# Kernel optimization log

Hardware: AMD Instinct MI355X
Metric: run time of the kernel (lower is better)

## Reference

```python
import jax, jax.numpy as jnp
import numpy as np

N = 100000
E = 1600000
L = 128   # latent_size
H = 128   # hidden_size
O = 128   # output_size


def setup_inputs() -> dict:
    key = jax.random.key(0)
    ks = jax.random.split(key, 16)
    s = 1.0 / np.sqrt(H)
    inp = {
        "z": jax.random.normal(ks[0], (N, L), dtype=jnp.float32),
        "edge_index": jax.random.randint(ks[1], (2, E), 0, N, dtype=jnp.int64),
        # LSTM params (torch order: i, f, g, o)
        "W_ih": jax.random.uniform(ks[2], (4 * H, L), jnp.float32, -s, s),
        "W_hh": jax.random.uniform(ks[3], (4 * H, H), jnp.float32, -s, s),
        "b_ih": jax.random.uniform(ks[4], (4 * H,), jnp.float32, -s, s),
        "b_hh": jax.random.uniform(ks[5], (4 * H,), jnp.float32, -s, s),
        # GCNConv weights (x @ W + b)
        "W1": jax.random.uniform(ks[6], (H, H), jnp.float32, -s, s),
        "b1": jnp.zeros((H,), jnp.float32),
        "W2": jax.random.uniform(ks[7], (H, H), jnp.float32, -s, s),
        "b2": jnp.zeros((H,), jnp.float32),
        # final Linear
        "W3": jax.random.uniform(ks[8], (O, H), jnp.float32, -s, s),
        "b3": jax.random.uniform(ks[9], (O,), jnp.float32, -s, s),
    }
    return inp


def _gcn_conv(x, W, b, src, dst, norm, n_nodes):
    # x: [N, H]; src/dst/norm: [E+N] (self-loops included)
    h = x @ W                                   # [N, H] transform first (H==H)
    msg = h[src] * norm[:, None]                # gather + edge scale
    out = jax.ops.segment_sum(msg, dst, num_segments=n_nodes)  # scatter-add
    return out + b


def _lstm_step(z, W_ih, W_hh, b_ih, b_hh):
    # single time-step, h0 = c0 = 0
    gates = z @ W_ih.T + (jnp.zeros((1, H), z.dtype) @ W_hh.T) + b_ih + b_hh
    i, f, g, o = jnp.split(gates, 4, axis=-1)
    c = jax.nn.sigmoid(i) * jnp.tanh(g)         # f * c0 == 0
    return jax.nn.sigmoid(o) * jnp.tanh(c)


def reference(z, edge_index, W_ih, W_hh, b_ih, b_hh, W1, b1, W2, b2, W3, b3):
    n = z.shape[0]
    # add self-loops (PyG GCNConv default)
    loop = jnp.arange(n, dtype=edge_index.dtype)
    src = jnp.concatenate([edge_index[0], loop])
    dst = jnp.concatenate([edge_index[1], loop])
    # symmetric normalization: deg from dst (incoming, incl. self-loop)
    deg = jax.ops.segment_sum(jnp.ones_like(dst, dtype=z.dtype), dst, num_segments=n)
    dinv = jnp.where(deg > 0, jax.lax.rsqrt(deg), 0.0)
    norm = dinv[src] * dinv[dst]

    h = _lstm_step(z, W_ih, W_hh, b_ih, b_hh)
    x = jax.nn.relu(_gcn_conv(h, W1, b1, src, dst, norm, n))
    x = _gcn_conv(x, W2, b2, src, dst, norm, n)
    return jax.nn.relu(x @ W3.T + b3)
```

## Files before the change

kernel.cpp:

```cpp
#include <hip/hip_runtime.h>
#include <math.h>

typedef __attribute__((ext_vector_type(8))) short short8;
typedef __attribute__((ext_vector_type(4))) float floatx4;

#define HDIM 128
#define NPB 256
#define BKMAX 1024
#define CHUNK 8192
#define STAGE_CAP 8192

__device__ __forceinline__ float bf2f(unsigned short u) {
    unsigned int x = ((unsigned int)u) << 16;
    float f;
    __builtin_memcpy(&f, &x, 4);
    return f;
}
__device__ __forceinline__ unsigned short f2bf(float f) {
    unsigned int x;
    __builtin_memcpy(&x, &f, 4);
    unsigned int r = (x + 0x7fffu + ((x >> 16) & 1u)) >> 16;
    return (unsigned short)r;
}
__device__ __forceinline__ void split1(float v, unsigned short& hi, unsigned short& lo) {
    unsigned int x;
    __builtin_memcpy(&x, &v, 4);
    hi = (unsigned short)(x >> 16);
    lo = f2bf(v - bf2f(hi));
}
__device__ __forceinline__ float fast_sigmoid(float x) {
    return 1.0f / (1.0f + __expf(-x));
}
__device__ __forceinline__ float fast_tanh(float x) {
    float ax = fabsf(x);
    float e = __expf(2.0f * ax);
    float t = 1.0f - 2.0f / (e + 1.0f);
    return copysignf(t, x);
}

__device__ __forceinline__ void gload_lds16(const void* g, void* lds) {
    __builtin_amdgcn_global_load_lds(
        (const __attribute__((address_space(1))) unsigned int*)g,
        (__attribute__((address_space(3))) unsigned int*)lds, 16, 0, 0);
}

__global__ void prep_weights_kernel(const float* __restrict__ Wih,
                                    const float* __restrict__ W1,
                                    const float* __restrict__ bih,
                                    const float* __restrict__ bhh,
                                    unsigned short* __restrict__ Wihh, unsigned short* __restrict__ Wihl,
                                    unsigned short* __restrict__ W1h,  unsigned short* __restrict__ W1l,
                                    float* __restrict__ bsum) {
    int i = blockIdx.x * 256 + threadIdx.x;
    unsigned short h, l;
    if (i < 65536) {
        split1(Wih[i], h, l);
        Wihh[i] = h; Wihl[i] = l;
    } else if (i < 81920) {
        int t = i - 65536, r = t >> 7, c = t & 127;
        split1(W1[r * HDIM + c], h, l);
        W1h[c * HDIM + r] = h; W1l[c * HDIM + r] = l;
    } else if (i < 82432) {
        int t = i - 81920;
        bsum[t] = bih[t] + bhh[t];
    }
}

__global__ void prep_w23_kernel(const float* __restrict__ W2,
                                const float* __restrict__ W3,
                                const float* __restrict__ b2,
                                const float* __restrict__ b3,
                                unsigned short* __restrict__ W23h,
                                unsigned short* __restrict__ W23l,
                                float* __restrict__ b23) {
    int i = blockIdx.x * 256 + threadIdx.x;
    if (i < 16384) {
        int n = i >> 7, k = i & 127;
        float s = 0.0f;
#pragma unroll 8
        for (int p = 0; p < 128; ++p)
            s += W2[k * HDIM + p] * W3[n * HDIM + p];
        unsigned short h, l;
        split1(s, h, l);
        W23h[n * HDIM + k] = h;
        W23l[n * HDIM + k] = l;
    } else if (i < 16512) {
        int n = i - 16384;
        float s = b3[n];
#pragma unroll 8
        for (int p = 0; p < 128; ++p)
            s += b2[p] * W3[n * HDIM + p];
        b23[n] = s;
    }
}

__global__ __launch_bounds__(256)
void bucket_hist_kernel(const int* __restrict__ ei, int* __restrict__ bcnt,
                        long E, int K) {
    __shared__ int h[BKMAX];
    const int tid = threadIdx.x;
    for (int i = tid; i < K; i += 256) h[i] = 0;
    __syncthreads();
    const long base = (long)blockIdx.x * CHUNK;
#pragma unroll
    for (int j = 0; j < CHUNK / 256; ++j) {
        long e = base + j * 256 + tid;
        if (e < E) atomicAdd(&h[((unsigned)ei[E + e]) >> 8], 1);
    }
    __syncthreads();
    for (int i = tid; i < K; i += 256) {
        int c = h[i];
        if (c) atomicAdd(&bcnt[i], c);
    }
}

__global__ __launch_bounds__(1024)
void scan_buckets_kernel(const int* __restrict__ bcnt, int* __restrict__ gbase,
                         int* __restrict__ gcur, int* __restrict__ offs,
                         int K, int N, int Etot) {
    __shared__ int buf[1024];
    const int t = threadIdx.x;
    const int v = (t < K) ? bcnt[t] : 0;
    buf[t] = v;
    __syncthreads();
    for (int off = 1; off < 1024; off <<= 1) {
        int x = buf[t];
        int y = (t >= off) ? buf[t - off] : 0;
        __syncthreads();
        buf[t] = x + y;
        __syncthreads();
    }
    if (t < K) { gbase[t] = buf[t] - v; gcur[t] = buf[t] - v; }
    if (t == 0) { gbase[K] = Etot; offs[N] = Etot; }
}

__global__ __launch_bounds__(256)
void pair_scatter_kernel(const int* __restrict__ ei, int* __restrict__ gcur,
                         unsigned int* __restrict__ pairs, long E, int K) {
    __shared__ int h[BKMAX];
    __shared__ int cur[BKMAX];
    const int tid = threadIdx.x;
    for (int i = tid; i < K; i += 256) h[i] = 0;
    __syncthreads();
    const long base = (long)blockIdx.x * CHUNK;
#pragma unroll
    for (int j = 0; j < CHUNK / 256; ++j) {
        long e = base + j * 256 + tid;
        if (e < E) atomicAdd(&h[((unsigned)ei[E + e]) >> 8], 1);
    }
    __syncthreads();
    for (int i = tid; i < K; i += 256) {
        int c = h[i];
        cur[i] = c ? atomicAdd(&gcur[i], c) : 0;
    }
    __syncthreads();
#pragma unroll
    for (int j = 0; j < CHUNK / 256; ++j) {
        long e = base + j * 256 + tid;
        if (e < E) {
            unsigned int s = (unsigned int)ei[e];
            unsigned int d = (unsigned int)ei[E + e];
            int b = d >> 8;
            int pos = atomicAdd(&cur[b], 1);
            pairs[pos] = s | ((d & (NPB - 1)) << 24);
        }
    }
}

__global__ __launch_bounds__(256)
void bucket_csr_kernel(const unsigned int* __restrict__ pairs, const int* __restrict__ gbase,
                       int* __restrict__ offs, float* __restrict__ dinv,
                       int* __restrict__ srclist, int N) {
    __shared__ int cnt[NPB];
    __shared__ int red[NPB];
    __shared__ int cur[NPB];
    __shared__ int stage[STAGE_CAP];
    const int tid = threadIdx.x;
    const int b = blockIdx.x;
    const int node0 = b << 8;
    const int nn = min(NPB, N - node0);
    const int ebeg = gbase[b];
    const int eend = gbase[b + 1];
    const int ne = eend - ebeg;

    cnt[tid] = 0;
    __syncthreads();
    for (int i = tid; i < ne; i += 256)
        atomicAdd(&cnt[pairs[ebeg + i] >> 24], 1);
    __syncthreads();
    const int myc = cnt[tid];
    red[tid] = myc;
    __syncthreads();
    for (int off = 1; off < NPB; off <<= 1) {
        int x = red[tid];
        int y = (tid >= off) ? red[tid - off] : 0;
        __syncthreads();
        red[tid] = x + y;
        __syncthreads();
    }
    const int loff = red[tid] - myc;
    if (tid < nn) {
        offs[node0 + tid] = ebeg + loff;
        dinv[node0 + tid] = rsqrtf((float)myc + 1.0f);
    }
    cur[tid] = loff;
    __syncthreads();

    if (ne <= STAGE_CAP) {
        for (int i = tid; i < ne; i += 256) {
            unsigned int p = pairs[ebeg + i];
            int pos = atomicAdd(&cur[p >> 24], 1);
            stage[pos] = (int)(p & 0xFFFFFFu);
        }
        __syncthreads();
        for (int i = tid; i < ne; i += 256)
            srclist[ebeg + i] = stage[i];
    } else {
        for (int i = tid; i < ne; i += 256) {
            unsigned int p = pairs[ebeg + i];
            int pos = atomicAdd(&cur[p >> 24], 1);
            srclist[ebeg + pos] = (int)(p & 0xFFFFFFu);
        }
    }
}

__device__ __forceinline__ void stage_swz(const unsigned short* __restrict__ g,
                                          long rowBase, long maxRow, int kOff,
                                          unsigned short* lds, int nrows, int tid) {
    const int nchunks = nrows << 3;
    for (int L = tid; L < nchunks; L += 256) {
        int r = L >> 3, cS = L & 7;
        int cG = cS ^ (r & 7);
        long gr = rowBase + r;
        if (gr >= maxRow) gr = maxRow - 1;
        gload_lds16(g + gr * HDIM + kOff + cG * 8, lds + (long)L * 8);
    }
}
__device__ __forceinline__ int swz_off(int r, int c0) {
    return (r * 8 + (c0 ^ (r & 7))) * 8;
}

__global__ __launch_bounds__(256, 4)
void gemm_split(const unsigned short* __restrict__ Ah, const unsigned short* __restrict__ Al,
                const unsigned short* __restrict__ Bh, const unsigned short* __restrict__ Bl,
                float* __restrict__ outf, unsigned short* __restrict__ outb, long M,
                const float* __restrict__ rowScale,
                const float* __restrict__ bias, int mode)
{
    __shared__ unsigned short sBh[128 * 64], sBl[128 * 64];
    const int tid = threadIdx.x;
    const long rowBase = (long)blockIdx.x * 64;

    const int wave = tid >> 6;
    const int lane = tid & 63;
    const int quad = lane >> 4;
    const int l16  = lane & 15;
    const int arow = wave * 16 + l16;
    long ag = rowBase + arow;
    if (ag >= M) ag = M - 1;

    short8 rah[2][2], ral[2][2];
#pragma unroll
    for (int h = 0; h < 2; ++h)
#pragma unroll
        for (int kk = 0; kk < 2; ++kk) {
            const long o = ag * HDIM + h * 64 + kk * 32 + quad * 8;
            rah[h][kk] = *(const short8*)(Ah + o);
            ral[h][kk] = *(const short8*)(Al + o);
        }

    floatx4 acc[8];
#pragma unroll
    for (int i = 0; i < 8; ++i) acc[i] = (floatx4)0.0f;

    for (int h = 0; h < 2; ++h) {
        __syncthreads();
        stage_swz(Bh, 0, 128, h * 64, sBh, 128, tid);
        stage_swz(Bl, 0, 128, h * 64, sBl, 128, tid);
        __syncthreads();
#pragma unroll
        for (int kk = 0; kk < 2; ++kk) {
            const int c0 = kk * 4 + quad;
            short8 ah = rah[h][kk];
            short8 al = ral[h][kk];
#pragma unroll
            for (int ct = 0; ct < 8; ++ct) {
                const int bo = swz_off(ct * 16 + l16, c0);
                short8 bh = *(const short8*)(sBh + bo);
                short8 bl = *(const short8*)(sBl + bo);
                acc[ct] = __builtin_amdgcn_mfma_f32_16x16x32_bf16(ah, bh, acc[ct], 0, 0, 0);
                acc[ct] = __builtin_amdgcn_mfma_f32_16x16x32_bf16(ah, bl, acc[ct], 0, 0, 0);
                acc[ct] = __builtin_amdgcn_mfma_f32_16x16x32_bf16(al, bh, acc[ct], 0, 0, 0);
            }
        }
    }

#pragma unroll
    for (int ct = 0; ct < 8; ++ct) {
#pragma unroll
        for (int r = 0; r < 4; ++r) {
            long m = rowBase + wave * 16 + quad * 4 + r;
            if (m < M) {
                int n = ct * 16 + l16;
                float v = acc[ct][r];
                if (mode == 0) {
                    v *= rowScale[m];
                    outb[m * HDIM + n] = f2bf(v);
                } else {
                    v += bias[n];
                    v = fmaxf(v, 0.0f);
                    outf[m * HDIM + n] = v;
                }
            }
        }
    }
}

__global__ __launch_bounds__(256, 2)
void lstm_gemm1_fused(const float* __restrict__ Z,
                      const unsigned short* __restrict__ Wh, const unsigned short* __restrict__ Wl,
                      const unsigned short* __restrict__ W1h, const unsigned short* __restrict__ W1l,
                      const float* __restrict__ bsum, const float* __restrict__ dinv,
                      unsigned short* __restrict__ Tb, long M)
{
    __shared__ unsigned short sBh[2][128 * 64], sBl[2][128 * 64];
    const int tid = threadIdx.x;
    const long rowBase = (long)blockIdx.x * 64;

    const int wave = tid >> 6;
    const int lane = tid & 63;
    const int quad = lane >> 4;
    const int l16  = lane & 15;
    const int arow = wave * 16 + l16;
    long ag = rowBase + arow;
    if (ag >= M) ag = M - 1;

    short8 rah[2][2], ral[2][2];
#pragma unroll
    for (int h = 0; h < 2; ++h)
#pragma unroll
        for (int kk = 0; kk < 2; ++kk) {
            const float* p = Z + ag * HDIM + h * 64 + kk * 32 + quad * 8;
            float4 f0 = *(const float4*)p;
            float4 f1 = *(const float4*)(p + 4);
            float f[8] = {f0.x, f0.y, f0.z, f0.w, f1.x, f1.y, f1.z, f1.w};
#pragma unroll
            for (int e = 0; e < 8; ++e) {
                unsigned short hi, lo;
                split1(f[e], hi, lo);
                rah[h][kk][e] = (short)hi;
                ral[h][kk][e] = (short)lo;
            }
        }

    auto stage_phase = [&](int ph, int b) {
        const int g = ph >> 1, h = ph & 1;
        const int gateRow = (g == 0) ? 0 : ((g == 1) ? 256 : 384);
        const unsigned short* gh = Wh + (long)gateRow * HDIM + h * 64;
        const unsigned short* gl = Wl + (long)gateRow * HDIM + h * 64;
#pragma unroll
        for (int it = 0; it < 4; ++it) {
            int L = it * 256 + tid;
            int r = L >> 3, cS = L & 7, cG = cS ^ (r & 7);
            gload_lds16(gh + (long)r * HDIM + cG * 8, &sBh[b][L * 8]);
        }
#pragma unroll
        for (int it = 0; it < 4; ++it) {
            int L = it * 256 + tid;
            int r = L >> 3, cS = L & 7, cG = cS ^ (r & 7);
            gload_lds16(gl + (long)r * HDIM + cG * 8, &sBl[b][L * 8]);
        }
    };

    floatx4 acc[8];
    floatx4 st[8];
#pragma unroll
    for (int i = 0; i < 8; ++i) acc[i] = (floatx4)0.0f;

    stage_phase(0, 0);

#pragma unroll
    for (int ph = 0; ph < 6; ++ph) {
        const int b = ph & 1;
        if (ph < 5) stage_phase(ph + 1, b ^ 1);
        if (ph == 2) {
#pragma unroll
            for (int ct = 0; ct < 8; ++ct) {
                const float bb = bsum[ct * 16 + l16];
#pragma unroll
                for (int r = 0; r < 4; ++r)
                    st[ct][r] = fast_sigmoid(acc[ct][r] + bb);
                acc[ct] = (floatx4)0.0f;
            }
        } else if (ph == 4) {
#pragma unroll
            for (int ct = 0; ct < 8; ++ct) {
                const float bb = bsum[256 + ct * 16 + l16];
#pragma unroll
                for (int r = 0; r < 4; ++r) {
                    float cv = st[ct][r] * fast_tanh(acc[ct][r] + bb);
                    st[ct][r] = fast_tanh(cv);
                }
                acc[ct] = (floatx4)0.0f;
            }
        }
        if (ph < 5) asm volatile("s_waitcnt vmcnt(8)" ::: "memory");
        else        asm volatile("s_waitcnt vmcnt(0)" ::: "memory");
        __builtin_amdgcn_s_barrier();
        asm volatile("" ::: "memory");
        const int hh_ = ph & 1;
#pragma unroll
        for (int kk = 0; kk < 2; ++kk) {
            const int c0 = kk * 4 + quad;
            short8 a_h = rah[hh_][kk];
            short8 a_l = ral[hh_][kk];
#pragma unroll
            for (int ct = 0; ct < 8; ++ct) {
                const int bo = swz_off(ct * 16 + l16, c0);
                short8 bh = *(const short8*)(&sBh[b][0] + bo);
                short8 bl = *(const short8*)(&sBl[b][0] + bo);
                acc[ct] = __builtin_amdgcn_mfma_f32_16x16x32_bf16(a_h, bh, acc[ct], 0, 0, 0);
                acc[ct] = __builtin_amdgcn_mfma_f32_16x16x32_bf16(a_h, bl, acc[ct], 0, 0, 0);
                acc[ct] = __builtin_amdgcn_mfma_f32_16x16x32_bf16(a_l, bh, acc[ct], 0, 0, 0);
            }
        }
        asm volatile("s_waitcnt lgkmcnt(0)" ::: "memory");
        __builtin_amdgcn_s_barrier();
        asm volatile("" ::: "memory");
    }

#pragma unroll
    for (int ct = 0; ct < 8; ++ct) {
        const float bb = bsum[384 + ct * 16 + l16];
#pragma unroll
        for (int r = 0; r < 4; ++r) {
            float hv = fast_sigmoid(acc[ct][r] + bb) * st[ct][r];
            unsigned short hh, hl;
            split1(hv, hh, hl);
            int row = wave * 16 + quad * 4 + r;
            int col = ct * 16 + l16;
            int c = col >> 3;
            int sc = (c & 8) | ((c ^ row) & 7);
            int idx = (row * 16 + sc) * 8 + (col & 7);
            sBh[0][idx] = hh;
            sBl[0][idx] = hl;
        }
    }

    floatx4 acc2[8];
#pragma unroll
    for (int i = 0; i < 8; ++i) acc2[i] = (floatx4)0.0f;

#pragma unroll
    for (int h2 = 0; h2 < 2; ++h2) {
        __syncthreads();
        stage_swz(W1h, 0, 128, h2 * 64, &sBh[1][0], 128, tid);
        stage_swz(W1l, 0, 128, h2 * 64, &sBl[1][0], 128, tid);
        __syncthreads();
#pragma unroll
        for (int kk = 0; kk < 2; ++kk) {
            const int cA = h2 * 8 + kk * 4 + quad;
            const int scA = (cA & 8) | ((cA ^ arow) & 7);
            short8 a_h = *(const short8*)(&sBh[0][(arow * 16 + scA) * 8]);
            short8 a_l = *(const short8*)(&sBl[0][(arow * 16 + scA) * 8]);
            const int c0 = kk * 4 + quad;
#pragma unroll
            for (int ct = 0; ct < 8; ++ct) {
                const int bo = swz_off(ct * 16 + l16, c0);
                short8 bh = *(const short8*)(&sBh[1][0] + bo);
                short8 bl = *(const short8*)(&sBl[1][0] + bo);
                acc2[ct] = __builtin_amdgcn_mfma_f32_16x16x32_bf16(a_h, bh, acc2[ct], 0, 0, 0);
                acc2[ct] = __builtin_amdgcn_mfma_f32_16x16x32_bf16(a_h, bl, acc2[ct], 0, 0, 0);
                acc2[ct] = __builtin_amdgcn_mfma_f32_16x16x32_bf16(a_l, bh, acc2[ct], 0, 0, 0);
            }
        }
    }

#pragma unroll
    for (int ct = 0; ct < 8; ++ct) {
#pragma unroll
        for (int r = 0; r < 4; ++r) {
            long m = rowBase + wave * 16 + quad * 4 + r;
            if (m < M) {
                int n = ct * 16 + l16;
                float v = acc2[ct][r] * dinv[m];
                Tb[m * HDIM + n] = f2bf(v);
            }
        }
    }
}

__global__ __launch_bounds__(256, 4)
void aggregate_kernel(const unsigned short* __restrict__ t, const int* __restrict__ srclist,
                      const int* __restrict__ offs, const float* __restrict__ dinv,
                      const float* __restrict__ bias, int doRelu,
                      unsigned short* __restrict__ Xh, unsigned short* __restrict__ Xl,
                      float* __restrict__ outF, long N)
{
    long node = (long)blockIdx.x * 4 + (threadIdx.x >> 6);
    if (node >= N) return;
    const int lane = threadIdx.x & 63;
    const int c = lane * 2;
    const int beg = offs[node];
    const int end = offs[node + 1];
    float s0[8], s1[8];
#pragma unroll
    for (int q = 0; q < 8; ++q) { s0[q] = 0.0f; s1[q] = 0.0f; }
    int j = beg;
    for (; j + 8 <= end; j += 8) {
        int srcs[8];
#pragma unroll
        for (int q = 0; q < 8; ++q) srcs[q] = srclist[j + q];
        unsigned int p[8];
#pragma unroll
        for (int q = 0; q < 8; ++q) p[q] = *(const unsigned int*)(t + (long)srcs[q] * HDIM + c);
#pragma unroll
        for (int q = 0; q < 8; ++q) {
            s0[q] += bf2f((unsigned short)(p[q] & 0xffffu));
            s1[q] += bf2f((unsigned short)(p[q] >> 16));
        }
    }
    for (; j + 4 <= end; j += 4) {
        int srcs[4];
#pragma unroll
        for (int q = 0; q < 4; ++q) srcs[q] = srclist[j + q];
#pragma unroll
        for (int q = 0; q < 4; ++q) {
            unsigned int p = *(const unsigned int*)(t + (long)srcs[q] * HDIM + c);
            s0[q] += bf2f((unsigned short)(p & 0xffffu));
            s1[q] += bf2f((unsigned short)(p >> 16));
        }
    }
    for (; j < end; ++j) {
        unsigned int p = *(const unsigned int*)(t + (long)srclist[j] * HDIM + c);
        s0[0] += bf2f((unsigned short)(p & 0xffffu));
        s1[0] += bf2f((unsigned short)(p >> 16));
    }
    const unsigned int ps = *(const unsigned int*)(t + node * HDIM + c);
    s0[0] += bf2f((unsigned short)(ps & 0xffffu));
    s1[0] += bf2f((unsigned short)(ps >> 16));
    float a0 = ((s0[0] + s0[1]) + (s0[2] + s0[3])) + ((s0[4] + s0[5]) + (s0[6] + s0[7]));
    float a1 = ((s1[0] + s1[1]) + (s1[2] + s1[3])) + ((s1[4] + s1[5]) + (s1[6] + s1[7]));
    const float d = dinv[node];
    float v0 = d * a0 + bias[c];
    float v1 = d * a1 + bias[c + 1];
    if (outF) {
        v0 = fmaxf(v0, 0.0f);
        v1 = fmaxf(v1, 0.0f);
        float2 o2 = {v0, v1};
        *(float2*)(outF + node * HDIM + c) = o2;
        return;
    }
    if (doRelu) { v0 = fmaxf(v0, 0.0f); v1 = fmaxf(v1, 0.0f); }
    unsigned short h0, l0, h1, l1;
    split1(v0, h0, l0);
    split1(v1, h1, l1);
    *(unsigned int*)(Xh + node * HDIM + c) = (unsigned int)h0 | ((unsigned int)h1 << 16);
    *(unsigned int*)(Xl + node * HDIM + c) = (unsigned int)l0 | ((unsigned int)l1 << 16);
}

extern "C" void kernel_launch(void* const* d_in, const int* in_sizes, int n_in,
                              void* d_out, int out_size, void* d_ws, size_t ws_size,
                              hipStream_t stream)
{
    const float* z   = (const float*)d_in[0];
    const int*   ei  = (const int*)d_in[1];
    const float* Wih = (const float*)d_in[2];
    const float* bih = (const float*)d_in[4];
    const float* bhh = (const float*)d_in[5];
    const float* W1  = (const float*)d_in[6];
    const float* b1  = (const float*)d_in[7];
    const float* W2  = (const float*)d_in[8];
    const float* b2  = (const float*)d_in[9];
    const float* W3  = (const float*)d_in[10];
    const float* b3  = (const float*)d_in[11];
    float* out = (float*)d_out;

    const long N = in_sizes[0] / HDIM;
    const long E = in_sizes[1] / 2;
    const int  K = (int)((N + NPB - 1) / NPB);

    char* ws = (char*)d_ws;
    size_t off = 0;
    auto alloc = [&](size_t bytes) {
        char* p = ws + off;
        off += (bytes + 255) & ~(size_t)255;
        return (void*)p;
    };
    int*   bcnt    = (int*)alloc(K * 4);
    int*   gbase   = (int*)alloc((K + 1) * 4);
    int*   gcur    = (int*)alloc(K * 4);
    int*   offs    = (int*)alloc((N + 1) * 4);
    float* dinv    = (float*)alloc(N * 4);
    unsigned int* pairs = (unsigned int*)alloc(E * 4);
    int*   srclist = (int*)alloc(E * 4);
    unsigned short* P1h = (unsigned short*)alloc(N * HDIM * 2);
    unsigned short* P1l = (unsigned short*)alloc(N * HDIM * 2);
    unsigned short* Tb  = (unsigned short*)alloc(N * HDIM * 2);
    unsigned short* Wihh = (unsigned short*)alloc(512 * HDIM * 2);
    unsigned short* Wihl = (unsigned short*)alloc(512 * HDIM * 2);
    unsigned short* W1h  = (unsigned short*)alloc(HDIM * HDIM * 2);
    unsigned short* W1l  = (unsigned short*)alloc(HDIM * HDIM * 2);
    unsigned short* W23h = (unsigned short*)alloc(HDIM * HDIM * 2);
    unsigned short* W23l = (unsigned short*)alloc(HDIM * HDIM * 2);
    float* bsum = (float*)alloc(512 * 4);
    float* b23  = (float*)alloc(HDIM * 4);

    const int gblocks  = (int)((N + 63) / 64);
    const int ablocks  = (int)((N + 3) / 4);
    const int cblocks  = (int)((E + CHUNK - 1) / CHUNK);

    hipMemsetAsync(bcnt, 0, K * 4, stream);
    bucket_hist_kernel<<<cblocks, 256, 0, stream>>>(ei, bcnt, E, K);
    scan_buckets_kernel<<<1, 1024, 0, stream>>>(bcnt, gbase, gcur, offs, K, (int)N, (int)E);
    pair_scatter_kernel<<<cblocks, 256, 0, stream>>>(ei, gcur, pairs, E, K);
    bucket_csr_kernel<<<K, 256, 0, stream>>>(pairs, gbase, offs, dinv, srclist, (int)N);

    prep_weights_kernel<<<322, 256, 0, stream>>>(Wih, W1, bih, bhh,
                                                 Wihh, Wihl, W1h, W1l, bsum);
    prep_w23_kernel<<<65, 256, 0, stream>>>(W2, W3, b2, b3, W23h, W23l, b23);

    lstm_gemm1_fused<<<gblocks, 256, 0, stream>>>(z, Wihh, Wihl, W1h, W1l,
                                                  bsum, dinv, Tb, N);

    aggregate_kernel<<<ablocks, 256, 0, stream>>>(Tb, srclist, offs, dinv, b1, 1,
                                                  P1h, P1l, nullptr, N);

    gemm_split<<<gblocks, 256, 0, stream>>>(P1h, P1l, W23h, W23l, nullptr, Tb, N, dinv, nullptr, 0);
    aggregate_kernel<<<ablocks, 256, 0, stream>>>(Tb, srclist, offs, dinv, b23, 1,
                                                  nullptr, nullptr, out, N);
}
```

Baseline: 420.4 us.

## Fuse first GCN aggregation with second GEMM through LDS

Replaces the separate aggregate kernel and split-bf16 GEMM with one kernel. Each block gathers neighbour rows for its 64 nodes, applies bias and ReLU, splits the result into hi/lo bf16 in a swizzled LDS tile, then runs the MFMA GEMM against W23 directly. This removes the write and re-read of the two N×128 bf16 intermediate buffers and one kernel launch. In exchange the gather phase now runs with fewer blocks, each wave processing 16 nodes sequentially, and the higher LDS use lowers occupancy, which may weaken latency hiding for the irregular gathers.

```diff
diff --git a/kernel.cpp b/kernel.cpp
--- a/kernel.cpp
+++ b/kernel.cpp
@@ -240,82 +240,6 @@
     return (r * 8 + (c0 ^ (r & 7))) * 8;
 }
 
-__global__ __launch_bounds__(256, 4)
-void gemm_split(const unsigned short* __restrict__ Ah, const unsigned short* __restrict__ Al,
-                const unsigned short* __restrict__ Bh, const unsigned short* __restrict__ Bl,
-                float* __restrict__ outf, unsigned short* __restrict__ outb, long M,
-                const float* __restrict__ rowScale,
-                const float* __restrict__ bias, int mode)
-{
-    __shared__ unsigned short sBh[128 * 64], sBl[128 * 64];
-    const int tid = threadIdx.x;
-    const long rowBase = (long)blockIdx.x * 64;
-
-    const int wave = tid >> 6;
-    const int lane = tid & 63;
-    const int quad = lane >> 4;
-    const int l16  = lane & 15;
-    const int arow = wave * 16 + l16;
-    long ag = rowBase + arow;
-    if (ag >= M) ag = M - 1;
-
-    short8 rah[2][2], ral[2][2];
-#pragma unroll
-    for (int h = 0; h < 2; ++h)
-#pragma unroll
-        for (int kk = 0; kk < 2; ++kk) {
-            const long o = ag * HDIM + h * 64 + kk * 32 + quad * 8;
-            rah[h][kk] = *(const short8*)(Ah + o);
-            ral[h][kk] = *(const short8*)(Al + o);
-        }
-
-    floatx4 acc[8];
-#pragma unroll
-    for (int i = 0; i < 8; ++i) acc[i] = (floatx4)0.0f;
-
-    for (int h = 0; h < 2; ++h) {
-        __syncthreads();
-        stage_swz(Bh, 0, 128, h * 64, sBh, 128, tid);
-        stage_swz(Bl, 0, 128, h * 64, sBl, 128, tid);
-        __syncthreads();
-#pragma unroll
-        for (int kk = 0; kk < 2; ++kk) {
-            const int c0 = kk * 4 + quad;
-            short8 ah = rah[h][kk];
-            short8 al = ral[h][kk];
-#pragma unroll
-            for (int ct = 0; ct < 8; ++ct) {
-                const int bo = swz_off(ct * 16 + l16, c0);
-                short8 bh = *(const short8*)(sBh + bo);
-                short8 bl = *(const short8*)(sBl + bo);
-                acc[ct] = __builtin_amdgcn_mfma_f32_16x16x32_bf16(ah, bh, acc[ct], 0, 0, 0);
-                acc[ct] = __builtin_amdgcn_mfma_f32_16x16x32_bf16(ah, bl, acc[ct], 0, 0, 0);
-                acc[ct] = __builtin_amdgcn_mfma_f32_16x16x32_bf16(al, bh, acc[ct], 0, 0, 0);
-            }
-        }
-    }
-
-#pragma unroll
-    for (int ct = 0; ct < 8; ++ct) {
-#pragma unroll
-        for (int r = 0; r < 4; ++r) {
-            long m = rowBase + wave * 16 + quad * 4 + r;
-            if (m < M) {
-                int n = ct * 16 + l16;
-                float v = acc[ct][r];
-                if (mode == 0) {
-                    v *= rowScale[m];
-                    outb[m * HDIM + n] = f2bf(v);
-                } else {
-                    v += bias[n];
-                    v = fmaxf(v, 0.0f);
-                    outf[m * HDIM + n] = v;
-                }
-            }
-        }
-    }
-}
-
 __global__ __launch_bounds__(256, 2)
 void lstm_gemm1_fused(const float* __restrict__ Z,
                       const unsigned short* __restrict__ Wh, const unsigned short* __restrict__ Wl,
@@ -485,6 +409,127 @@
                 int n = ct * 16 + l16;
                 float v = acc2[ct][r] * dinv[m];
                 Tb[m * HDIM + n] = f2bf(v);
+            }
+        }
+    }
+}
+
+__global__ __launch_bounds__(256, 2)
+void agg1_gemm2_fused(const unsigned short* __restrict__ t, const int* __restrict__ srclist,
+                      const int* __restrict__ offs, const float* __restrict__ dinv,
+                      const float* __restrict__ b1,
+                      const unsigned short* __restrict__ Bh, const unsigned short* __restrict__ Bl,
+                      unsigned short* __restrict__ Tb2, long M)
+{
+    __shared__ unsigned short sAh[64 * 128], sAl[64 * 128];
+    __shared__ unsigned short sBh[128 * 64], sBl[128 * 64];
+    const int tid = threadIdx.x;
+    const long rowBase = (long)blockIdx.x * 64;
+
+    const int wave = tid >> 6;
+    const int lane = tid & 63;
+    const int quad = lane >> 4;
+    const int l16  = lane & 15;
+
+    const int c = lane * 2;
+    for (int i = 0; i < 16; ++i) {
+        const int row = wave * 16 + i;
+        const long node = rowBase + row;
+        float v0 = 0.0f, v1 = 0.0f;
+        if (node < M) {
+            const int beg = offs[node];
+            const int end = offs[node + 1];
+            float s0[8], s1[8];
+#pragma unroll
+            for (int q = 0; q < 8; ++q) { s0[q] = 0.0f; s1[q] = 0.0f; }
+            int j = beg;
+            for (; j + 8 <= end; j += 8) {
+                int srcs[8];
+#pragma unroll
+                for (int q = 0; q < 8; ++q) srcs[q] = srclist[j + q];
+                unsigned int p[8];
+#pragma unroll
+                for (int q = 0; q < 8; ++q) p[q] = *(const unsigned int*)(t + (long)srcs[q] * HDIM + c);
+#pragma unroll
+                for (int q = 0; q < 8; ++q) {
+                    s0[q] += bf2f((unsigned short)(p[q] & 0xffffu));
+                    s1[q] += bf2f((unsigned short)(p[q] >> 16));
+                }
+            }
+            for (; j + 4 <= end; j += 4) {
+                int srcs[4];
+#pragma unroll
+                for (int q = 0; q < 4; ++q) srcs[q] = srclist[j + q];
+#pragma unroll
+                for (int q = 0; q < 4; ++q) {
+                    unsigned int p = *(const unsigned int*)(t + (long)srcs[q] * HDIM + c);
+                    s0[q] += bf2f((unsigned short)(p & 0xffffu));
+                    s1[q] += bf2f((unsigned short)(p >> 16));
+                }
+            }
+            for (; j < end; ++j) {
+                unsigned int p = *(const unsigned int*)(t + (long)srclist[j] * HDIM + c);
+                s0[0] += bf2f((unsigned short)(p & 0xffffu));
+                s1[0] += bf2f((unsigned short)(p >> 16));
+            }
+            const unsigned int ps = *(const unsigned int*)(t + node * HDIM + c);
+            s0[0] += bf2f((unsigned short)(ps & 0xffffu));
+            s1[0] += bf2f((unsigned short)(ps >> 16));
+            float a0 = ((s0[0] + s0[1]) + (s0[2] + s0[3])) + ((s0[4] + s0[5]) + (s0[6] + s0[7]));
+            float a1 = ((s1[0] + s1[1]) + (s1[2] + s1[3])) + ((s1[4] + s1[5]) + (s1[6] + s1[7]));
+            const float d = dinv[node];
+            v0 = fmaxf(d * a0 + b1[c], 0.0f);
+            v1 = fmaxf(d * a1 + b1[c + 1], 0.0f);
+        }
+        unsigned short h0, l0, h1, l1;
+        split1(v0, h0, l0);
+        split1(v1, h1, l1);
+        const int ch = c >> 3;
+        const int sc = (ch & 8) | ((ch ^ row) & 7);
+        const int idx = (row * 16 + sc) * 8 + (c & 7);
+        *(unsigned int*)(sAh + idx) = (unsigned int)h0 | ((unsigned int)h1 << 16);
+        *(unsigned int*)(sAl + idx) = (unsigned int)l0 | ((unsigned int)l1 << 16);
+    }
+
+    const int arow = wave * 16 + l16;
+    floatx4 acc2[8];
+#pragma unroll
+    for (int i = 0; i < 8; ++i) acc2[i] = (floatx4)0.0f;
+
+#pragma unroll
+    for (int h2 = 0; h2 < 2; ++h2) {
+        __syncthreads();
+        stage_swz(Bh, 0, 128, h2 * 64, sBh, 128, tid);
+        stage_swz(Bl, 0, 128, h2 * 64, sBl, 128, tid);
+        __syncthreads();
+#pragma unroll
+        for (int kk = 0; kk < 2; ++kk) {
+            const int cA = h2 * 8 + kk * 4 + quad;
+            const int scA = (cA & 8) | ((cA ^ arow) & 7);
+            short8 a_h = *(const short8*)(&sAh[(arow * 16 + scA) * 8]);
+            short8 a_l = *(const short8*)(&sAl[(arow * 16 + scA) * 8]);
+            const int c0 = kk * 4 + quad;
+#pragma unroll
+            for (int ct = 0; ct < 8; ++ct) {
+                const int bo = swz_off(ct * 16 + l16, c0);
+                short8 bh = *(const short8*)(sBh + bo);
+                short8 bl = *(const short8*)(sBl + bo);
+                acc2[ct] = __builtin_amdgcn_mfma_f32_16x16x32_bf16(a_h, bh, acc2[ct], 0, 0, 0);
+                acc2[ct] = __builtin_amdgcn_mfma_f32_16x16x32_bf16(a_h, bl, acc2[ct], 0, 0, 0);
+                acc2[ct] = __builtin_amdgcn_mfma_f32_16x16x32_bf16(a_l, bh, acc2[ct], 0, 0, 0);
+            }
+        }
+    }
+
+#pragma unroll
+    for (int ct = 0; ct < 8; ++ct) {
+#pragma unroll
+        for (int r = 0; r < 4; ++r) {
+            long m = rowBase + wave * 16 + quad * 4 + r;
+            if (m < M) {
+                int n = ct * 16 + l16;
+                float v = acc2[ct][r] * dinv[m];
+                Tb2[m * HDIM + n] = f2bf(v);
             }
         }
     }
@@ -594,9 +639,8 @@
     float* dinv    = (float*)alloc(N * 4);
     unsigned int* pairs = (unsigned int*)alloc(E * 4);
     int*   srclist = (int*)alloc(E * 4);
-    unsigned short* P1h = (unsigned short*)alloc(N * HDIM * 2);
-    unsigned short* P1l = (unsigned short*)alloc(N * HDIM * 2);
     unsigned short* Tb  = (unsigned short*)alloc(N * HDIM * 2);
+    unsigned short* Tb2 = (unsigned short*)alloc(N * HDIM * 2);
     unsigned short* Wihh = (unsigned short*)alloc(512 * HDIM * 2);
     unsigned short* Wihl = (unsigned short*)alloc(512 * HDIM * 2);
     unsigned short* W1h  = (unsigned short*)alloc(HDIM * HDIM * 2);
@@ -623,10 +667,9 @@
     lstm_gemm1_fused<<<gblocks, 256, 0, stream>>>(z, Wihh, Wihl, W1h, W1l,
                                                   bsum, dinv, Tb, N);
 
-    aggregate_kernel<<<ablocks, 256, 0, stream>>>(Tb, srclist, offs, dinv, b1, 1,
-                                                  P1h, P1l, nullptr, N);
-
-    gemm_split<<<gblocks, 256, 0, stream>>>(P1h, P1l, W23h, W23l, nullptr, Tb, N, dinv, nullptr, 0);
-    aggregate_kernel<<<ablocks, 256, 0, stream>>>(Tb, srclist, offs, dinv, b23, 1,
+    agg1_gemm2_fused<<<gblocks, 256, 0, stream>>>(Tb, srclist, offs, dinv, b1,
+                                                  W23h, W23l, Tb2, N);
+
+    aggregate_kernel<<<ablocks, 256, 0, stream>>>(Tb2, srclist, offs, dinv, b23, 1,
                                                   nullptr, nullptr, out, N);
 }
```

Measured after the change: 530.4 us. +26.2%, slower.
